# Optimization experiments

Hardware: AMD Instinct MI355X
Metric: run time of the kernel (lower is better)

The kernel has to match this reference:

```python
import jax, jax.numpy as jnp
import numpy as np

WINDOW_SIZE = 11
N_CHANNELS = 3
SIGMA = 1.5
K1, K2 = 0.01, 0.03
VALUE_RANGE = 1.0


def _create_window(window_size: int, n_channels: int, sigma: float) -> np.ndarray:
    # 1D gaussian, normalized, then outer product -> 2D kernel
    coords = np.arange(window_size, dtype=np.float32) - (window_size - 1) / 2.0
    g = np.exp(-(coords ** 2) / (2.0 * sigma ** 2))
    g = g / g.sum()
    k2d = np.outer(g, g).astype(np.float32)  # (K, K), sums to 1
    # depthwise kernel, OIHW with I=1 (groups = n_channels)
    return np.broadcast_to(k2d, (n_channels, 1, window_size, window_size)).copy()


def _dwconv(x, window):
    # depthwise valid conv, NCHW / OIHW
    return jax.lax.conv_general_dilated(
        x, window, window_strides=(1, 1), padding='VALID',
        feature_group_count=window.shape[0],
        dimension_numbers=('NCHW', 'OIHW', 'NCHW'))


def setup_inputs() -> dict:
    key = jax.random.key(0)
    kx, ky = jax.random.split(key)
    N, C, H, W = 32, N_CHANNELS, 512, 512
    x = jax.random.uniform(kx, (N, C, H, W), dtype=jnp.float32)
    y = jax.random.uniform(ky, (N, C, H, W), dtype=jnp.float32)
    window = jnp.asarray(_create_window(WINDOW_SIZE, N_CHANNELS, SIGMA))
    return {"x": x, "y": y, "window": window}


def reference(x, y, window):
    c1 = (K1 * VALUE_RANGE) ** 2
    c2 = (K2 * VALUE_RANGE) ** 2

    mu_x = _dwconv(x, window)
    mu_y = _dwconv(y, window)
    mu_x_sq = mu_x ** 2
    mu_y_sq = mu_y ** 2
    mu_xy = mu_x * mu_y

    sigma_x_sq = _dwconv(x * x, window) - mu_x_sq
    sigma_y_sq = _dwconv(y * y, window) - mu_y_sq
    sigma_xy = _dwconv(x * y, window) - mu_xy

    cs = (2.0 * sigma_xy + c2) / (sigma_x_sq + sigma_y_sq + c2)
    ss = (2.0 * mu_xy + c1) / (mu_x_sq + mu_y_sq + c1) * cs

    l = ss.mean(axis=(-1, -2))  # (N, C) per-channel SSIM
    l = l.mean(axis=-1)         # (N,)  per-sample
    return l.mean()             # reduction='mean'
```

## Files before the change

kernel.cpp:

```cpp
#include <hip/hip_runtime.h>

typedef float v2f __attribute__((ext_vector_type(2)));

#define KS    11
#define HH    512
#define WW    512
#define OUTD  502
#define GR    11
#define NG    5
#define ROWS  55
#define OH    45
#define NBR   12
#define NBC   2
#define TC    256
#define SGQ   134
#define SGL   268
#define NIMG  96
#define ITEMS (GR * SGQ)
#define NIT   6

__global__ __launch_bounds__(256, 3)
void ssim_main(const float* __restrict__ xg, const float* __restrict__ yg,
               const float* __restrict__ win, double* __restrict__ acc_out)
{
    __shared__ v2f buf[2][GR][SGL];
    __shared__ float wsums[4];

    const int tid = threadIdx.x;
    int bb = blockIdx.x;
    const int img  = bb % NIMG;  bb /= NIMG;
    const int band = bb % NBR;   bb /= NBR;
    const int cb   = bb * TC;
    const int row0 = band * OH;

    float g[KS];
    #pragma unroll
    for (int i = 0; i < KS; i++) {
        float s = 0.f;
        #pragma unroll
        for (int j = 0; j < KS; j++) s += win[i * KS + j];
        g[i] = s;
    }

    const float* xi = xg + (size_t)img * (HH * WW);
    const float* yi = yg + (size_t)img * (HH * WW);

    float2 pfx[NIT], pfy[NIT];
    auto prefetch = [&](int gidx) {
        #pragma unroll
        for (int it = 0; it < NIT; it++) {
            const int idx = tid + 256 * it;
            if (idx < ITEMS) {
                int i = idx / SGQ, k = idx - i * SGQ;
                int gr = row0 + gidx * GR + i; if (gr > HH - 1) gr = HH - 1;
                int gc = cb + 2 * k;           if (gc > WW - 2) gc = WW - 2;
                const size_t base = (size_t)gr * WW + gc;
                pfx[it] = *(const float2*)(xi + base);
                pfy[it] = *(const float2*)(yi + base);
            }
        }
    };
    auto store_s = [&](int bsel) {
        #pragma unroll
        for (int it = 0; it < NIT; it++) {
            const int idx = tid + 256 * it;
            if (idx < ITEMS) {
                int i = idx / SGQ, k = idx - i * SGQ;
                float4 w; w.x = pfx[it].x; w.y = pfy[it].x;
                          w.z = pfx[it].y; w.w = pfy[it].y;
                *(float4*)&buf[bsel][i][2 * k] = w;
            }
        }
    };

    float rh[4][KS];
    #pragma unroll
    for (int q = 0; q < 4; q++)
        #pragma unroll
        for (int s = 0; s < KS; s++) rh[q][s] = 0.f;

    float ssum = 0.f;
    const float C1 = 0.0001f;
    const float C2 = 0.0009f;
    const bool colvalid = (cb + tid) < OUTD;

    auto hpass = [&](const v2f* rowp, int rr) {
        float hx = 0.f, hy = 0.f, hs = 0.f, hp = 0.f;
        #pragma unroll
        for (int j = 0; j < KS; j++) {
            const v2f v = rowp[j];
            const float s = fmaf(v.y, v.y, v.x * v.x);
            const float p = v.x * v.y;
            hx = fmaf(g[j], v.x, hx);
            hy = fmaf(g[j], v.y, hy);
            hs = fmaf(g[j], s,   hs);
            hp = fmaf(g[j], p,   hp);
        }
        rh[0][rr] = hx; rh[1][rr] = hy; rh[2][rr] = hs; rh[3][rr] = hp;
    };
    auto vpass = [&](int rr, int jout) {
        float mx = 0.f, my = 0.f, S = 0.f, P = 0.f;
        #pragma unroll
        for (int i = 0; i < KS; i++) {
            const int sl = (rr + 1 + i) % KS;
            mx = fmaf(g[i], rh[0][sl], mx);
            my = fmaf(g[i], rh[1][sl], my);
            S  = fmaf(g[i], rh[2][sl], S);
            P  = fmaf(g[i], rh[3][sl], P);
        }
        if (jout < OUTD && colvalid) {
            const float mxx = mx * mx, myy = my * my, mxy = mx * my;
            const float ssig = S - mxx - myy;
            const float sxy  = P - mxy;
            const float num = (2.f * mxy + C1) * (2.f * sxy + C2);
            const float den = (mxx + myy + C1) * (ssig + C2);
            float rc = __builtin_amdgcn_rcpf(den);
            rc = rc * fmaf(-den, rc, 2.0f);
            ssum = fmaf(num, rc, ssum);
        }
    };

    prefetch(0); store_s(0); prefetch(1);
    __syncthreads();

    {
        store_s(1);
        prefetch(2);
        const v2f (*bufc)[SGL] = buf[0];
        #pragma unroll
        for (int rr = 0; rr < GR; rr++) {
            hpass(&bufc[rr][tid], rr);
            if (rr == GR - 1) vpass(rr, row0);
        }
        __syncthreads();
    }
    #pragma unroll 1
    for (int gi = 1; gi < NG; gi++) {
        if (gi + 1 < NG) store_s((gi + 1) & 1);
        if (gi + 2 < NG) prefetch(gi + 2);
        const v2f (*bufc)[SGL] = buf[gi & 1];
        const int jbase = row0 + gi * GR - (KS - 1);
        #pragma unroll
        for (int rr = 0; rr < GR; rr++) {
            hpass(&bufc[rr][tid], rr);
            vpass(rr, jbase + rr);
        }
        __syncthreads();
    }

    #pragma unroll
    for (int off = 32; off > 0; off >>= 1)
        ssum += __shfl_down(ssum, off);
    const int wave = tid >> 6;
    if ((tid & 63) == 0) wsums[wave] = ssum;
    __syncthreads();
    if (tid == 0) {
        float s = wsums[0] + wsums[1] + wsums[2] + wsums[3];
        atomicAdd(acc_out, (double)s);
    }
}

__global__ void ssim_finalize(const double* __restrict__ acc, float* __restrict__ out)
{
    out[0] = (float)(acc[0] * (1.0 / 24192384.0));
}

extern "C" void kernel_launch(void* const* d_in, const int* in_sizes, int n_in,
                              void* d_out, int out_size, void* d_ws, size_t ws_size,
                              hipStream_t stream)
{
    const float* x   = (const float*)d_in[0];
    const float* y   = (const float*)d_in[1];
    const float* win = (const float*)d_in[2];
    float* out = (float*)d_out;
    double* acc = (double*)d_ws;

    hipMemsetAsync(acc, 0, sizeof(double), stream);
    ssim_main<<<dim3(NIMG * NBR * NBC), dim3(256), 0, stream>>>(x, y, win, acc);
    ssim_finalize<<<dim3(1), dim3(1), 0, stream>>>(acc, out);
}
```

Baseline: 316.9 us.

## Load tiles straight into LDS with global_load_lds instead of register staging

```diff
diff --git a/kernel.cpp b/kernel.cpp
--- a/kernel.cpp
+++ b/kernel.cpp
@@ -1,6 +1,4 @@
 #include <hip/hip_runtime.h>
-
-typedef float v2f __attribute__((ext_vector_type(2)));
 
 #define KS    11
 #define HH    512
@@ -8,22 +6,25 @@
 #define OUTD  502
 #define GR    11
 #define NG    5
-#define ROWS  55
 #define OH    45
 #define NBR   12
 #define NBC   2
 #define TC    256
-#define SGQ   134
-#define SGL   268
+#define ROWF  272
+#define CHK   68
+#define QTOT  (GR * CHK)
+#define GFL   3072
 #define NIMG  96
-#define ITEMS (GR * SGQ)
-#define NIT   6
+
+#define AS1 __attribute__((address_space(1)))
+#define AS3 __attribute__((address_space(3)))
 
 __global__ __launch_bounds__(256, 3)
 void ssim_main(const float* __restrict__ xg, const float* __restrict__ yg,
                const float* __restrict__ win, double* __restrict__ acc_out)
 {
-    __shared__ v2f buf[2][GR][SGL];
+    __shared__ float xbuf[2][GFL];
+    __shared__ float ybuf[2][GFL];
     __shared__ float wsums[4];
 
     const int tid = threadIdx.x;
@@ -45,31 +46,18 @@
     const float* xi = xg + (size_t)img * (HH * WW);
     const float* yi = yg + (size_t)img * (HH * WW);
 
-    float2 pfx[NIT], pfy[NIT];
-    auto prefetch = [&](int gidx) {
+    auto dma_group = [&](int gidx, int bsel) {
         #pragma unroll
-        for (int it = 0; it < NIT; it++) {
-            const int idx = tid + 256 * it;
-            if (idx < ITEMS) {
-                int i = idx / SGQ, k = idx - i * SGQ;
-                int gr = row0 + gidx * GR + i; if (gr > HH - 1) gr = HH - 1;
-                int gc = cb + 2 * k;           if (gc > WW - 2) gc = WW - 2;
-                const size_t base = (size_t)gr * WW + gc;
-                pfx[it] = *(const float2*)(xi + base);
-                pfy[it] = *(const float2*)(yi + base);
-            }
-        }
-    };
-    auto store_s = [&](int bsel) {
-        #pragma unroll
-        for (int it = 0; it < NIT; it++) {
-            const int idx = tid + 256 * it;
-            if (idx < ITEMS) {
-                int i = idx / SGQ, k = idx - i * SGQ;
-                float4 w; w.x = pfx[it].x; w.y = pfy[it].x;
-                          w.z = pfx[it].y; w.w = pfy[it].y;
-                *(float4*)&buf[bsel][i][2 * k] = w;
-            }
+        for (int it = 0; it < 3; it++) {
+            const int q = tid + 256 * it;
+            int i = q / CHK, k = q - i * CHK;
+            int gr = row0 + gidx * GR + i; if (gr > HH - 1) gr = HH - 1;
+            int gc = cb + 4 * k;           if (gc > WW - 4) gc = WW - 4;
+            const size_t gofs = (size_t)gr * WW + gc;
+            __builtin_amdgcn_global_load_lds(
+                (AS1 const void*)(xi + gofs), (AS3 void*)&xbuf[bsel][4 * q], 16, 0, 0);
+            __builtin_amdgcn_global_load_lds(
+                (AS1 const void*)(yi + gofs), (AS3 void*)&ybuf[bsel][4 * q], 16, 0, 0);
         }
     };
 
@@ -84,65 +72,65 @@
     const float C2 = 0.0009f;
     const bool colvalid = (cb + tid) < OUTD;
 
-    auto hpass = [&](const v2f* rowp, int rr) {
+    auto hpass = [&](const float* Xr, const float* Yr, int rr) {
         float hx = 0.f, hy = 0.f, hs = 0.f, hp = 0.f;
         #pragma unroll
         for (int j = 0; j < KS; j++) {
-            const v2f v = rowp[j];
-            const float s = fmaf(v.y, v.y, v.x * v.x);
-            const float p = v.x * v.y;
-            hx = fmaf(g[j], v.x, hx);
-            hy = fmaf(g[j], v.y, hy);
-            hs = fmaf(g[j], s,   hs);
-            hp = fmaf(g[j], p,   hp);
+            const float xj = Xr[j], yj = Yr[j];
+            hx = fmaf(g[j], xj, hx);
+            hy = fmaf(g[j], yj, hy);
+            hs = fmaf(g[j], fmaf(xj, xj, yj * yj), hs);
+            hp = fmaf(g[j], xj * yj, hp);
         }
         rh[0][rr] = hx; rh[1][rr] = hy; rh[2][rr] = hs; rh[3][rr] = hp;
     };
     auto vpass = [&](int rr, int jout) {
-        float mx = 0.f, my = 0.f, S = 0.f, P = 0.f;
-        #pragma unroll
-        for (int i = 0; i < KS; i++) {
-            const int sl = (rr + 1 + i) % KS;
-            mx = fmaf(g[i], rh[0][sl], mx);
-            my = fmaf(g[i], rh[1][sl], my);
-            S  = fmaf(g[i], rh[2][sl], S);
-            P  = fmaf(g[i], rh[3][sl], P);
-        }
-        if (jout < OUTD && colvalid) {
-            const float mxx = mx * mx, myy = my * my, mxy = mx * my;
-            const float ssig = S - mxx - myy;
-            const float sxy  = P - mxy;
-            const float num = (2.f * mxy + C1) * (2.f * sxy + C2);
-            const float den = (mxx + myy + C1) * (ssig + C2);
-            float rc = __builtin_amdgcn_rcpf(den);
-            rc = rc * fmaf(-den, rc, 2.0f);
-            ssum = fmaf(num, rc, ssum);
+        if (jout < OUTD) {
+            float mx = 0.f, my = 0.f, S = 0.f, P = 0.f;
+            #pragma unroll
+            for (int i = 0; i < KS; i++) {
+                const int sl = (rr + 1 + i) % KS;
+                mx = fmaf(g[i], rh[0][sl], mx);
+                my = fmaf(g[i], rh[1][sl], my);
+                S  = fmaf(g[i], rh[2][sl], S);
+                P  = fmaf(g[i], rh[3][sl], P);
+            }
+            if (colvalid) {
+                const float mxx = mx * mx, myy = my * my, mxy = mx * my;
+                const float ssig = S - mxx - myy;
+                const float sxy  = P - mxy;
+                const float num = (2.f * mxy + C1) * (2.f * sxy + C2);
+                const float den = (mxx + myy + C1) * (ssig + C2);
+                float rc = __builtin_amdgcn_rcpf(den);
+                rc = rc * fmaf(-den, rc, 2.0f);
+                ssum = fmaf(num, rc, ssum);
+            }
         }
     };
 
-    prefetch(0); store_s(0); prefetch(1);
+    dma_group(0, 0);
     __syncthreads();
 
     {
-        store_s(1);
-        prefetch(2);
-        const v2f (*bufc)[SGL] = buf[0];
+        dma_group(1, 1);
+        const float* X = &xbuf[0][0];
+        const float* Y = &ybuf[0][0];
         #pragma unroll
         for (int rr = 0; rr < GR; rr++) {
-            hpass(&bufc[rr][tid], rr);
+            hpass(X + rr * ROWF + tid, Y + rr * ROWF + tid, rr);
             if (rr == GR - 1) vpass(rr, row0);
         }
         __syncthreads();
     }
     #pragma unroll 1
     for (int gi = 1; gi < NG; gi++) {
-        if (gi + 1 < NG) store_s((gi + 1) & 1);
-        if (gi + 2 < NG) prefetch(gi + 2);
-        const v2f (*bufc)[SGL] = buf[gi & 1];
+        if (gi + 1 < NG) dma_group(gi + 1, (gi + 1) & 1);
+        const float* X = &xbuf[gi & 1][0];
+        const float* Y = &ybuf[gi & 1][0];
         const int jbase = row0 + gi * GR - (KS - 1);
         #pragma unroll
         for (int rr = 0; rr < GR; rr++) {
-            hpass(&bufc[rr][tid], rr);
+            hpass(X + rr * ROWF + tid, Y + rr * ROWF + tid, rr);
             vpass(rr, jbase + rr);
         }
         __syncthreads();
```

Result: faster. 290.1 us (-8.5%).
